# Kernel optimization log

Measured on AMD Instinct MI355X. Metric: run time of the kernel, lower is better.

The kernel has to match this reference:

```python
import jax, jax.numpy as jnp
import numpy as np

N_FEAT = 64
O_FEAT = 64
REDUCTION = 16


def conv2d(x, w, pad):
    # x: NCHW, w: OIHW
    return jax.lax.conv_general_dilated(
        x, w, window_strides=(1, 1), padding=[(pad, pad), (pad, pad)],
        dimension_numbers=('NCHW', 'OIHW', 'NCHW'))


def bwt(x):
    # Haar-like wavelet decompose: [B,C,H,W] -> [B,8C,H/2,W/2]
    x01 = x[:, :, 0::2, :] / 2
    x02 = x[:, :, 1::2, :] / 2
    x1 = x01[:, :, :, 0::2]
    x2 = x02[:, :, :, 0::2]
    x3 = x01[:, :, :, 1::2]
    x4 = x02[:, :, :, 1::2]
    x_LL = x1 + x2 + x3 + x4
    x_HL = -x1 - x2 + x3 + x4
    x_LH = -x1 + x2 - x3 + x4
    x_HH = x1 - x2 - x3 + x4
    x_HD = x1 + x2 - x3 - x4
    x_LV = -x1 + x2 + x3 - x4
    x_LD = x1 - x2 + x3 - x4
    x_HV = -x1 - x2 - x3 - x4
    return jnp.concatenate((x_LL, x_HL, x_LH, x_HH, x_HD, x_LV, x_LD, x_HV), axis=1)


def ibwt(x):
    # [B,8C,h,w] -> [B,C,2h,2w]
    B, C8, h, w = x.shape
    C = C8 // 8
    xs = [x[:, i * C:(i + 1) * C] / 2 for i in range(8)]
    x1, x2, x3, x4, x5, x6, x7, x8 = xs
    a00 = x1 - x2 - x3 + x4 + x5 - x6 + x7 - x8  # h[0::2, 0::2]
    a10 = x1 - x2 + x3 - x4 - x5 + x6 - x7 + x8  # h[1::2, 0::2]
    a01 = x1 + x2 - x3 - x4 - x5 - x6 + x7 + x8  # h[0::2, 1::2]
    a11 = x1 + x2 + x3 + x4 + x5 + x6 + x7 + x8  # h[1::2, 1::2]
    # interleave columns then rows
    even_rows = jnp.stack([a00, a01], axis=-1).reshape(B, C, h, 2 * w)
    odd_rows = jnp.stack([a10, a11], axis=-1).reshape(B, C, h, 2 * w)
    return jnp.stack([even_rows, odd_rows], axis=-2).reshape(B, C, 2 * h, 2 * w)


def sal(x, w_sal):
    max_pool = jnp.max(x, axis=1, keepdims=True)
    avg_pool = jnp.mean(x, axis=1, keepdims=True)
    channel_pool = jnp.concatenate([max_pool, avg_pool], axis=1)
    y = jax.nn.sigmoid(conv2d(channel_pool, w_sal, pad=2))
    return x * y


def cal(x, w_ca1, w_ca2):
    y = jnp.mean(x, axis=(2, 3), keepdims=True)  # adaptive avg pool to 1x1
    y = jax.nn.relu(conv2d(y, w_ca1, pad=0))
    y = jax.nn.sigmoid(conv2d(y, w_ca2, pad=0))
    return x * y


def setup_inputs() -> dict:
    key = jax.random.key(0)
    ks = jax.random.split(key, 10)
    n, o, r = N_FEAT, O_FEAT, REDUCTION
    s = 0.05
    return {
        'x': jax.random.normal(ks[0], (4, n, 256, 256), dtype=jnp.float32),
        'w_body1': jax.random.normal(ks[1], (n, 8 * n, 3, 3), dtype=jnp.float32) * s,
        'w_body2': jax.random.normal(ks[2], (8 * n, n, 3, 3), dtype=jnp.float32) * s,
        'w_sal': jax.random.normal(ks[3], (1, 2, 5, 5), dtype=jnp.float32) * s,
        'w_ca1': jax.random.normal(ks[4], (8 * n // r, 8 * n, 1, 1), dtype=jnp.float32) * s,
        'w_ca2': jax.random.normal(ks[5], (8 * n, 8 * n // r, 1, 1), dtype=jnp.float32) * s,
        'w_1x1': jax.random.normal(ks[6], (8 * n, 8 * n, 1, 1), dtype=jnp.float32) * s,
        'w_3x3': jax.random.normal(ks[7], (o, n, 3, 3), dtype=jnp.float32) * s,
        'w_final': jax.random.normal(ks[8], (o, n, 1, 1), dtype=jnp.float32) * s,
    }


def reference(x, w_body1, w_body2, w_sal, w_ca1, w_ca2, w_1x1, w_3x3, w_final):
    residual = x
    x_bwt = bwt(x)                               # [B, 8n, H/2, W/2]
    res = conv2d(x_bwt, w_body1, pad=1)          # body: conv-act-conv
    res = jax.nn.relu(res)
    res = conv2d(res, w_body2, pad=1)
    res = sal(res, w_sal)
    res = cal(res, w_ca1, w_ca2)
    res = conv2d(res, w_1x1, pad=0) + x_bwt
    wavelet_path = ibwt(res)                     # [B, n, H, W]
    out = jax.nn.relu(conv2d(wavelet_path, w_3x3, pad=1))
    out = out + conv2d(residual, w_final, pad=0)
    return out
```

## Files before the change

kernel.cpp:

```cpp
#include <hip/hip_runtime.h>
#include <hip/hip_bf16.h>

typedef __hip_bfloat16 bf16;
using short8  = __attribute__((ext_vector_type(8))) short;
using floatx4 = __attribute__((ext_vector_type(4))) float;

__device__ __forceinline__ float b2f(bf16 v) { return __bfloat162float(v); }
__device__ __forceinline__ bf16 f2b(float v) { return __float2bfloat16(v); }
__device__ __forceinline__ float s2f(short s) {
    return __uint_as_float(((unsigned)(unsigned short)s) << 16);
}
__device__ __forceinline__ unsigned short fbits(float v) {
    bf16 b = f2b(v);
    return *(unsigned short*)&b;
}

constexpr int H = 256, W = 256, Hh = 128, Wh = 128, C8 = 512;
constexpr int HWh = Hh * Wh;
constexpr int HWf = H * W;
constexpr int ICP = 40;

template<int OC, int IC>
__global__ __launch_bounds__(256) void prep_wr(const float* __restrict__ w, bf16* __restrict__ wr) {
    int idx = blockIdx.x * 256 + threadIdx.x;
    if (idx >= 9 * OC * IC) return;
    int ic = idx & (IC - 1);
    int oc = (idx / IC) & (OC - 1);
    int tap = idx / (IC * OC);
    wr[idx] = f2b(w[(oc * IC + ic) * 9 + tap]);
}

__global__ __launch_bounds__(256) void prep_wfr(const float* __restrict__ wf, bf16* __restrict__ wfr) {
    int idx = blockIdx.x * 256 + threadIdx.x;
    wfr[idx] = f2b(wf[idx]);
}

__global__ __launch_bounds__(256) void prep_w1s(const float* __restrict__ w1,
                                                const float* __restrict__ scale,
                                                bf16* __restrict__ w1s) {
    int idx = blockIdx.x * 256 + threadIdx.x;
    int ic = idx & 511, oc = (idx >> 9) & 511, b = idx >> 18;
    w1s[idx] = f2b(w1[oc * 512 + ic] * scale[b * 512 + ic]);
}

constexpr int XROW = 130;
__global__ __launch_bounds__(256, 2) void bwt_nhwc(const float* __restrict__ x, bf16* __restrict__ A) {
    __shared__ unsigned short sX[2 * 64 * XROW];
    int bx = blockIdx.x;
    int i = bx >> 1, j0 = (bx & 1) * 64;
    int b = blockIdx.z;
    int tid = threadIdx.x;
    for (int k = 0; k < 16; k++) {
        int e = tid + k * 256;
        int w4 = e & 31, r = (e >> 5) & 1, c = e >> 6;
        float4 v = *(const float4*)(x + (((size_t)(b * 64 + c) * H + 2 * i + r) * W) + j0 * 2 + w4 * 4);
        unsigned lo = ((unsigned)fbits(v.y) << 16) | fbits(v.x);
        unsigned hi = ((unsigned)fbits(v.w) << 16) | fbits(v.z);
        unsigned short* dst = sX + (r * 64 + c) * XROW + w4 * 4;
        *(unsigned*)(dst) = lo;
        *(unsigned*)(dst + 2) = hi;
    }
    __syncthreads();
    int c = tid & 63, wid = tid >> 6;
    for (int k = 0; k < 16; k++) {
        int jr = wid * 16 + k;
        unsigned ev = *(const unsigned*)(sX + c * XROW + jr * 2);
        unsigned od = *(const unsigned*)(sX + (64 + c) * XROW + jr * 2);
        float x1 = s2f((short)(ev & 0xffff)) * 0.5f;
        float x3 = s2f((short)(ev >> 16)) * 0.5f;
        float x2 = s2f((short)(od & 0xffff)) * 0.5f;
        float x4 = s2f((short)(od >> 16)) * 0.5f;
        float v[8];
        v[0] =  x1 + x2 + x3 + x4;
        v[1] = -x1 - x2 + x3 + x4;
        v[2] = -x1 + x2 - x3 + x4;
        v[3] =  x1 - x2 - x3 + x4;
        v[4] =  x1 + x2 - x3 - x4;
        v[5] = -x1 + x2 + x3 - x4;
        v[6] =  x1 - x2 + x3 - x4;
        v[7] = -x1 - x2 - x3 - x4;
        size_t base = ((size_t)((b * Hh + i) * Wh) + j0 + jr) * 512 + c;
        #pragma unroll
        for (int band = 0; band < 8; band++)
            A[base + band * 64] = f2b(v[band]);
    }
}

template<int IC, int OC, int HW, bool RELU, int MINW>
__global__ __launch_bounds__(256, MINW) void conv3x3_mfma(const bf16* __restrict__ in,
                                                          const bf16* __restrict__ wr,
                                                          bf16* __restrict__ out) {
    __shared__ bf16 sIn[18 * 18 * ICP];
    __shared__ bf16 sW9[9 * 64 * ICP];

    const int tilesX = HW / 16;
    int tX = (blockIdx.x % tilesX) * 16;
    int tY = (blockIdx.x / tilesX) * 16;
    int oBase = blockIdx.y * 64;
    int b = blockIdx.z;
    int tid = threadIdx.x;
    int lane = tid & 63, wid = tid >> 6;
    int m = lane & 15, quad = lane >> 4;

    floatx4 acc[4][4];
    #pragma unroll
    for (int i = 0; i < 4; i++)
        #pragma unroll
        for (int j = 0; j < 4; j++)
            acc[i][j] = (floatx4){0.f, 0.f, 0.f, 0.f};

    const bf16* inB = in + (size_t)b * HW * HW * IC;

    for (int ic0 = 0; ic0 < IC; ic0 += 32) {
        __syncthreads();
        for (int e = tid; e < 18 * 18 * 4; e += 256) {
            int q = e & 3, cell = e >> 2;
            int r = cell / 18, c = cell - r * 18;
            int gr = tY + r - 1, gc = tX + c - 1;
            short8 v = {0, 0, 0, 0, 0, 0, 0, 0};
            if (gr >= 0 && gr < HW && gc >= 0 && gc < HW)
                v = *(const short8*)(inB + (size_t)(gr * HW + gc) * IC + ic0 + q * 8);
            *(short8*)(sIn + cell * ICP + q * 8) = v;
        }
        for (int e = tid; e < 2304; e += 256) {
            int q = e & 3, row = e >> 2;
            int tap = row >> 6, oc = row & 63;
            short8 v = *(const short8*)(wr + (size_t)(tap * OC + oBase + oc) * IC + ic0 + q * 8);
            *(short8*)(sW9 + row * ICP + q * 8) = v;
        }
        __syncthreads();
        #pragma unroll
        for (int dy = 0; dy < 3; dy++) {
            #pragma unroll
            for (int dx = 0; dx < 3; dx++) {
                short8 bfr[4];
                #pragma unroll
                for (int nt = 0; nt < 4; nt++)
                    bfr[nt] = *(const short8*)(sW9 + ((dy * 3 + dx) * 64 + nt * 16 + m) * ICP + quad * 8);
                #pragma unroll
                for (int mt = 0; mt < 4; mt++) {
                    int r = wid * 4 + mt;
                    short8 afr = *(const short8*)(sIn + ((r + dy) * 18 + m + dx) * ICP + quad * 8);
                    #pragma unroll
                    for (int nt = 0; nt < 4; nt++)
                        acc[mt][nt] = __builtin_amdgcn_mfma_f32_16x16x32_bf16(afr, bfr[nt], acc[mt][nt], 0, 0, 0);
                }
            }
        }
    }
    #pragma unroll
    for (int mt = 0; mt < 4; mt++) {
        int row = tY + wid * 4 + mt;
        #pragma unroll
        for (int nt = 0; nt < 4; nt++) {
            int oc = oBase + nt * 16 + m;
            #pragma unroll
            for (int reg = 0; reg < 4; reg++) {
                int col = tX + quad * 4 + reg;
                float v = acc[mt][nt][reg];
                if (RELU) v = fmaxf(v, 0.f);
                out[((size_t)(b * HW + row) * HW + col) * OC + oc] = f2b(v);
            }
        }
    }
}

__global__ __launch_bounds__(256, 2) void conv1x1_mfma(const bf16* __restrict__ t3,
                                                       const float* __restrict__ smap,
                                                       const bf16* __restrict__ w1s,
                                                       bf16* __restrict__ A) {
    __shared__ bf16 sX[256 * ICP];
    __shared__ bf16 sW1[128 * ICP];
    int p0 = blockIdx.x * 256;
    int oBase = blockIdx.y * 128;
    int b = blockIdx.z;
    int tid = threadIdx.x;
    int lane = tid & 63, wid = tid >> 6;
    int m = lane & 15, quad = lane >> 4;
    const bf16* wB = w1s + (size_t)b * 512 * 512;
    const bf16* tB = t3 + ((size_t)b << 14) * 512;
    const float* sm = smap + (b << 14);

    floatx4 acc[4][8];
    #pragma unroll
    for (int i = 0; i < 4; i++)
        #pragma unroll
        for (int j = 0; j < 8; j++)
            acc[i][j] = (floatx4){0.f, 0.f, 0.f, 0.f};

    for (int ic0 = 0; ic0 < 512; ic0 += 32) {
        __syncthreads();
        #pragma unroll
        for (int k = 0; k < 4; k++) {
            int e = tid + k * 256;
            int q = e & 3, p = e >> 2;
            float sc = sm[p0 + p];
            short8 v = *(const short8*)(tB + (size_t)(p0 + p) * 512 + ic0 + q * 8);
            short8 o;
            #pragma unroll
            for (int t = 0; t < 8; t++)
                o[t] = (short)fbits(s2f(v[t]) * sc);
            *(short8*)(sX + p * ICP + q * 8) = o;
        }
        #pragma unroll
        for (int k = 0; k < 2; k++) {
            int e = tid + k * 256;
            int q = e & 3, oc = e >> 2;
            *(short8*)(sW1 + oc * ICP + q * 8) =
                *(const short8*)(wB + (size_t)(oBase + oc) * 512 + ic0 + q * 8);
        }
        __syncthreads();
        short8 bfr[8];
        #pragma unroll
        for (int nt = 0; nt < 8; nt++)
            bfr[nt] = *(const short8*)(sW1 + (nt * 16 + m) * ICP + quad * 8);
        #pragma unroll
        for (int mt = 0; mt < 4; mt++) {
            short8 afr = *(const short8*)(sX + ((wid * 4 + mt) * 16 + m) * ICP + quad * 8);
            #pragma unroll
            for (int nt = 0; nt < 8; nt++)
                acc[mt][nt] = __builtin_amdgcn_mfma_f32_16x16x32_bf16(afr, bfr[nt], acc[mt][nt], 0, 0, 0);
        }
    }
    bf16* AB = A + ((size_t)b << 14) * 512;
    #pragma unroll
    for (int mt = 0; mt < 4; mt++) {
        #pragma unroll
        for (int nt = 0; nt < 8; nt++) {
            int oc = oBase + nt * 16 + m;
            #pragma unroll
            for (int reg = 0; reg < 4; reg++) {
                int p = p0 + wid * 64 + mt * 16 + quad * 4 + reg;
                size_t a = (size_t)p * 512 + oc;
                AB[a] = f2b(acc[mt][nt][reg] + b2f(AB[a]));
            }
        }
    }
}

__global__ __launch_bounds__(256) void sal_pool(const bf16* __restrict__ t2, float* __restrict__ pool) {
    int pix = blockIdx.x * 4 + (threadIdx.x >> 6);
    int lane = threadIdx.x & 63;
    short8 v = *(const short8*)(t2 + (size_t)pix * 512 + lane * 8);
    float mx = -1e30f, sm = 0.f;
    #pragma unroll
    for (int i = 0; i < 8; i++) {
        float f = s2f(v[i]);
        mx = fmaxf(mx, f);
        sm += f;
    }
    #pragma unroll
    for (int off = 32; off > 0; off >>= 1) {
        mx = fmaxf(mx, __shfl_xor(mx, off));
        sm += __shfl_xor(sm, off);
    }
    if (lane == 0) {
        int b = pix >> 14, px = pix & (HWh - 1);
        pool[((size_t)(b * 2) << 14) + px] = mx;
        pool[((size_t)(b * 2 + 1) << 14) + px] = sm * (1.f / 512.f);
    }
}

__global__ __launch_bounds__(256) void sal_conv(const float* __restrict__ pool,
                                                const float* __restrict__ wsal,
                                                float* __restrict__ smap) {
    int p = blockIdx.x * 256 + threadIdx.x;
    int b = p >> 14, px = p & (HWh - 1);
    int iy = px >> 7, ix = px & 127;
    float acc = 0.f;
    #pragma unroll
    for (int ch = 0; ch < 2; ch++)
        #pragma unroll
        for (int dy = 0; dy < 5; dy++)
            #pragma unroll
            for (int dx = 0; dx < 5; dx++) {
                int gy = iy + dy - 2, gx = ix + dx - 2;
                if (gy >= 0 && gy < Hh && gx >= 0 && gx < Wh)
                    acc += pool[((size_t)(b * 2 + ch) << 14) + gy * Wh + gx] *
                           wsal[ch * 25 + dy * 5 + dx];
            }
    smap[p] = 1.f / (1.f + expf(-acc));
}

__global__ __launch_bounds__(256) void sal_wsum(const bf16* __restrict__ t2,
                                                const float* __restrict__ smap,
                                                float* __restrict__ chsum) {
    int b = blockIdx.y;
    int p0 = blockIdx.x * 32;
    int t = threadIdx.x;
    float s0 = 0.f, s1 = 0.f;
    const bf16* tB = t2 + ((size_t)b << 14) * 512;
    #pragma unroll 4
    for (int k = 0; k < 32; k++) {
        int pix = p0 + k;
        float sc = smap[(b << 14) + pix];
        unsigned v = *(const unsigned*)(tB + (size_t)pix * 512 + 2 * t);
        s0 += s2f((short)(v & 0xffff)) * sc;
        s1 += s2f((short)(v >> 16)) * sc;
    }
    atomicAdd(&chsum[b * 512 + 2 * t], s0);
    atomicAdd(&chsum[b * 512 + 2 * t + 1], s1);
}

__global__ __launch_bounds__(512) void cal_kernel(const float* __restrict__ chsum,
                                                  const float* __restrict__ wca1,
                                                  const float* __restrict__ wca2,
                                                  float* __restrict__ scale) {
    int b = blockIdx.x;
    __shared__ float sMean[512];
    __shared__ float sH[32];
    sMean[threadIdx.x] = chsum[b * C8 + threadIdx.x] * (1.f / 16384.f);
    __syncthreads();
    if (threadIdx.x < 32) {
        float a = 0.f;
        for (int cc = 0; cc < 512; cc++)
            a += wca1[threadIdx.x * 512 + cc] * sMean[cc];
        sH[threadIdx.x] = fmaxf(a, 0.f);
    }
    __syncthreads();
    float a = 0.f;
    #pragma unroll
    for (int j = 0; j < 32; j++)
        a += wca2[threadIdx.x * 32 + j] * sH[j];
    scale[b * C8 + threadIdx.x] = 1.f / (1.f + expf(-a));
}

__global__ __launch_bounds__(256) void ibwt_nhwc(const bf16* __restrict__ A, bf16* __restrict__ E) {
    int idx = blockIdx.x * 256 + threadIdx.x;
    int c = idx & 63;
    int j = (idx >> 6) & 127;
    int i = (idx >> 13) & 127;
    int b = idx >> 20;
    size_t base = (size_t)(idx >> 6) * 512 + c;
    float xs[8];
    #pragma unroll
    for (int k = 0; k < 8; k++)
        xs[k] = b2f(A[base + k * 64]) * 0.5f;
    float a00 = xs[0] - xs[1] - xs[2] + xs[3] + xs[4] - xs[5] + xs[6] - xs[7];
    float a10 = xs[0] - xs[1] + xs[2] - xs[3] - xs[4] + xs[5] - xs[6] + xs[7];
    float a01 = xs[0] + xs[1] - xs[2] - xs[3] - xs[4] - xs[5] + xs[6] + xs[7];
    float a11 = xs[0] + xs[1] + xs[2] + xs[3] + xs[4] + xs[5] + xs[6] + xs[7];
    bf16* Ep = E + ((size_t)((b * H + 2 * i) * W + 2 * j)) * 64 + c;
    Ep[0]           = f2b(a00);
    Ep[64]          = f2b(a01);
    Ep[W * 64]      = f2b(a10);
    Ep[W * 64 + 64] = f2b(a11);
}

__global__ __launch_bounds__(256, 2) void final_mfma(const bf16* __restrict__ E,
                                                     const bf16* __restrict__ wr3,
                                                     const float* __restrict__ x,
                                                     const bf16* __restrict__ wfr,
                                                     float* __restrict__ out) {
    __shared__ bf16 sIn[18 * 18 * ICP];
    __shared__ bf16 sW9[9 * 64 * ICP];
    const int tilesX = W / 16;
    int tX = (blockIdx.x % tilesX) * 16;
    int tY = (blockIdx.x / tilesX) * 16;
    int b = blockIdx.z;
    int tid = threadIdx.x;
    int lane = tid & 63, wid = tid >> 6;
    int m = lane & 15, quad = lane >> 4;

    floatx4 acc[4][4];
    #pragma unroll
    for (int i = 0; i < 4; i++)
        #pragma unroll
        for (int j = 0; j < 4; j++)
            acc[i][j] = (floatx4){0.f, 0.f, 0.f, 0.f};

    const bf16* inB = E + (size_t)b * HWf * 64;
    for (int ic0 = 0; ic0 < 64; ic0 += 32) {
        __syncthreads();
        for (int e = tid; e < 18 * 18 * 4; e += 256) {
            int q = e & 3, cell = e >> 2;
            int r = cell / 18, c = cell - r * 18;
            int gr = tY + r - 1, gc = tX + c - 1;
            short8 v = {0, 0, 0, 0, 0, 0, 0, 0};
            if (gr >= 0 && gr < H && gc >= 0 && gc < W)
                v = *(const short8*)(inB + (size_t)(gr * W + gc) * 64 + ic0 + q * 8);
            *(short8*)(sIn + cell * ICP + q * 8) = v;
        }
        for (int e = tid; e < 2304; e += 256) {
            int q = e & 3, row = e >> 2;
            int tap = row >> 6, oc = row & 63;
            short8 v = *(const short8*)(wr3 + (size_t)(tap * 64 + oc) * 64 + ic0 + q * 8);
            *(short8*)(sW9 + row * ICP + q * 8) = v;
        }
        __syncthreads();
        #pragma unroll
        for (int dy = 0; dy < 3; dy++) {
            #pragma unroll
            for (int dx = 0; dx < 3; dx++) {
                short8 bfr[4];
                #pragma unroll
                for (int nt = 0; nt < 4; nt++)
                    bfr[nt] = *(const short8*)(sW9 + ((dy * 3 + dx) * 64 + nt * 16 + m) * ICP + quad * 8);
                #pragma unroll
                for (int mt = 0; mt < 4; mt++) {
                    int r = wid * 4 + mt;
                    short8 afr = *(const short8*)(sIn + ((r + dy) * 18 + m + dx) * ICP + quad * 8);
                    #pragma unroll
                    for (int nt = 0; nt < 4; nt++)
                        acc[mt][nt] = __builtin_amdgcn_mfma_f32_16x16x32_bf16(afr, bfr[nt], acc[mt][nt], 0, 0, 0);
                }
            }
        }
    }
    #pragma unroll
    for (int i = 0; i < 4; i++)
        #pragma unroll
        for (int j = 0; j < 4; j++)
            #pragma unroll
            for (int r = 0; r < 4; r++)
                acc[i][j][r] = fmaxf(acc[i][j][r], 0.f);

    for (int icc = 0; icc < 64; icc += 32) {
        __syncthreads();
        for (int e = tid; e < 2048; e += 256) {
            int c4 = e & 3, r = (e >> 2) & 15, ic = e >> 6;
            float4 v = *(const float4*)(x + ((size_t)(b * 64 + icc + ic) * H + tY + r) * W + tX + c4 * 4);
            bf16* dst = sIn + ((r + 1) * 18 + c4 * 4 + 1) * ICP + ic;
            dst[0]       = f2b(v.x);
            dst[ICP]     = f2b(v.y);
            dst[2 * ICP] = f2b(v.z);
            dst[3 * ICP] = f2b(v.w);
        }
        {
            int q = tid & 3, oc = tid >> 2;
            *(short8*)(sW9 + (64 + oc) * ICP + q * 8) =
                *(const short8*)(wfr + oc * 64 + icc + q * 8);
        }
        __syncthreads();
        short8 bfr[4];
        #pragma unroll
        for (int nt = 0; nt < 4; nt++)
            bfr[nt] = *(const short8*)(sW9 + (64 + nt * 16 + m) * ICP + quad * 8);
        #pragma unroll
        for (int mt = 0; mt < 4; mt++) {
            int r = wid * 4 + mt;
            short8 afr = *(const short8*)(sIn + ((r + 1) * 18 + m + 1) * ICP + quad * 8);
            #pragma unroll
            for (int nt = 0; nt < 4; nt++)
                acc[mt][nt] = __builtin_amdgcn_mfma_f32_16x16x32_bf16(afr, bfr[nt], acc[mt][nt], 0, 0, 0);
        }
    }
    #pragma unroll
    for (int mt = 0; mt < 4; mt++) {
        int gr = tY + wid * 4 + mt;
        #pragma unroll
        for (int nt = 0; nt < 4; nt++) {
            int oc = nt * 16 + m;
            *(floatx4*)(out + ((size_t)(b * 64 + oc) * H + gr) * W + tX + quad * 4) = acc[mt][nt];
        }
    }
}

extern "C" void kernel_launch(void* const* d_in, const int* in_sizes, int n_in,
                              void* d_out, int out_size, void* d_ws, size_t ws_size,
                              hipStream_t stream) {
    const float* x       = (const float*)d_in[0];
    const float* w_body1 = (const float*)d_in[1];
    const float* w_body2 = (const float*)d_in[2];
    const float* w_sal   = (const float*)d_in[3];
    const float* w_ca1   = (const float*)d_in[4];
    const float* w_ca2   = (const float*)d_in[5];
    const float* w_1x1   = (const float*)d_in[6];
    const float* w_3x3   = (const float*)d_in[7];
    const float* w_final = (const float*)d_in[8];

    char* ws = (char*)d_ws;
    bf16*  A     = (bf16*)(ws + 0);
    bf16*  T2    = (bf16*)(ws + 67108864);
    bf16*  T1    = (bf16*)(ws + 134217728);
    float* pool  = (float*)(ws + 134217728);
    float* smap  = (float*)(ws + 134742016);
    float* chsum = (float*)(ws + 135004160);
    float* scale = (float*)(ws + 135012352);
    bf16*  w1s   = (bf16*)(ws + 135020544);
    bf16*  wr3   = (bf16*)(ws + 137117696);
    bf16*  wfr   = (bf16*)(ws + 137191424);
    bf16*  E     = T2;
    bf16*  wr1   = (bf16*)d_out;
    bf16*  wr2   = (bf16*)((char*)d_out + 589824);

    prep_wr<64, 512><<<1152, 256, 0, stream>>>(w_body1, wr1);
    prep_wr<512, 64><<<1152, 256, 0, stream>>>(w_body2, wr2);
    bwt_nhwc<<<dim3(256, 1, 4), 256, 0, stream>>>(x, A);
    conv3x3_mfma<512, 64, 128, true, 1><<<dim3(64, 1, 4), 256, 0, stream>>>(A, wr1, T1);
    conv3x3_mfma<64, 512, 128, false, 2><<<dim3(64, 8, 4), 256, 0, stream>>>(T1, wr2, T2);
    sal_pool<<<16384, 256, 0, stream>>>(T2, pool);
    sal_conv<<<256, 256, 0, stream>>>(pool, w_sal, smap);
    hipMemsetAsync(chsum, 0, 4 * 512 * sizeof(float), stream);
    sal_wsum<<<dim3(512, 4), 256, 0, stream>>>(T2, smap, chsum);
    cal_kernel<<<4, 512, 0, stream>>>(chsum, w_ca1, w_ca2, scale);
    prep_w1s<<<4096, 256, 0, stream>>>(w_1x1, scale, w1s);
    prep_wr<64, 64><<<144, 256, 0, stream>>>(w_3x3, wr3);
    prep_wfr<<<16, 256, 0, stream>>>(w_final, wfr);
    conv1x1_mfma<<<dim3(64, 4, 4), 256, 0, stream>>>(T2, smap, w1s, A);
    ibwt_nhwc<<<16384, 256, 0, stream>>>(A, E);
    final_mfma<<<dim3(256, 1, 4), 256, 0, stream>>>(E, wr3, x, wfr, (float*)d_out);
}
```

Baseline: 478.7 us.

## Pre-swizzle weights into MFMA fragment order and double-buffer activation tiles

Weights are repacked into per-lane MFMA B-fragment layout so conv kernels read them straight from global/L2 instead of staging them in shared memory. Activation tiles are double-buffered, with register prefetch of the next K chunk overlapping the MFMA work, and A-fragment rows are reused across the dy taps. The first conv moves to 8-row tiles for more blocks, and the spatial-attention scale in the 1x1 conv moves from the input to the output epilogue. In exchange, weight fragments come from cache every iteration and register pressure goes up.

```diff
diff --git a/kernel.cpp b/kernel.cpp
--- a/kernel.cpp
+++ b/kernel.cpp
@@ -21,26 +21,47 @@
 constexpr int ICP = 40;
 
 template<int OC, int IC>
-__global__ __launch_bounds__(256) void prep_wr(const float* __restrict__ w, bf16* __restrict__ wr) {
+__global__ __launch_bounds__(256) void prep_wrT(const float* __restrict__ w, bf16* __restrict__ wrT) {
     int idx = blockIdx.x * 256 + threadIdx.x;
     if (idx >= 9 * OC * IC) return;
-    int ic = idx & (IC - 1);
-    int oc = (idx / IC) & (OC - 1);
-    int tap = idx / (IC * OC);
-    wr[idx] = f2b(w[(oc * IC + ic) * 9 + tap]);
-}
-
-__global__ __launch_bounds__(256) void prep_wfr(const float* __restrict__ wf, bf16* __restrict__ wfr) {
+    constexpr int G = OC / 64, KC = IC / 32;
+    int j = idx & 7;
+    int l = (idx >> 3) & 63;
+    int nt = (idx >> 9) & 3;
+    int rest = idx >> 11;
+    int g = rest % G;
+    int rest2 = rest / G;
+    int kc = rest2 % KC;
+    int tap = rest2 / KC;
+    int oc = g * 64 + nt * 16 + (l & 15);
+    int ic = kc * 32 + (l >> 4) * 8 + j;
+    wrT[idx] = f2b(w[(oc * IC + ic) * 9 + tap]);
+}
+
+__global__ __launch_bounds__(256) void prep_w1sT(const float* __restrict__ w1,
+                                                 const float* __restrict__ scale,
+                                                 bf16* __restrict__ w1sT) {
     int idx = blockIdx.x * 256 + threadIdx.x;
-    wfr[idx] = f2b(wf[idx]);
-}
-
-__global__ __launch_bounds__(256) void prep_w1s(const float* __restrict__ w1,
-                                                const float* __restrict__ scale,
-                                                bf16* __restrict__ w1s) {
+    int j = idx & 7;
+    int l = (idx >> 3) & 63;
+    int nt = (idx >> 9) & 7;
+    int g = (idx >> 12) & 3;
+    int kc = (idx >> 14) & 15;
+    int b = idx >> 18;
+    int oc = g * 128 + nt * 16 + (l & 15);
+    int ic = kc * 32 + (l >> 4) * 8 + j;
+    w1sT[idx] = f2b(w1[oc * 512 + ic] * scale[b * 512 + ic]);
+}
+
+__global__ __launch_bounds__(256) void prep_wfrT(const float* __restrict__ wf, bf16* __restrict__ wfrT) {
     int idx = blockIdx.x * 256 + threadIdx.x;
-    int ic = idx & 511, oc = (idx >> 9) & 511, b = idx >> 18;
-    w1s[idx] = f2b(w1[oc * 512 + ic] * scale[b * 512 + ic]);
+    int j = idx & 7;
+    int l = (idx >> 3) & 63;
+    int nt = (idx >> 9) & 3;
+    int kc = idx >> 11;
+    int oc = nt * 16 + (l & 15);
+    int ic = kc * 32 + (l >> 4) * 8 + j;
+    wfrT[idx] = f2b(wf[oc * 64 + ic]);
 }
 
 constexpr int XROW = 130;
@@ -86,74 +107,98 @@
     }
 }
 
-template<int IC, int OC, int HW, bool RELU, int MINW>
-__global__ __launch_bounds__(256, MINW) void conv3x3_mfma(const bf16* __restrict__ in,
-                                                          const bf16* __restrict__ wr,
-                                                          bf16* __restrict__ out) {
-    __shared__ bf16 sIn[18 * 18 * ICP];
-    __shared__ bf16 sW9[9 * 64 * ICP];
+template<int IC, int OC, int HW, int TR, bool RELU>
+__global__ __launch_bounds__(256, 2) void conv3x3_mfma(const bf16* __restrict__ in,
+                                                       const bf16* __restrict__ wrT,
+                                                       bf16* __restrict__ out) {
+    constexpr int MT = TR / 4, NKC = IC / 32, G = OC / 64;
+    constexpr int CELLS = (TR + 2) * 18;
+    constexpr int NLD = (CELLS * 4 + 255) / 256;
+    __shared__ bf16 sIn[2][CELLS * ICP];
 
     const int tilesX = HW / 16;
     int tX = (blockIdx.x % tilesX) * 16;
-    int tY = (blockIdx.x / tilesX) * 16;
-    int oBase = blockIdx.y * 64;
+    int tY = (blockIdx.x / tilesX) * TR;
+    int g = blockIdx.y;
     int b = blockIdx.z;
     int tid = threadIdx.x;
     int lane = tid & 63, wid = tid >> 6;
     int m = lane & 15, quad = lane >> 4;
 
-    floatx4 acc[4][4];
-    #pragma unroll
-    for (int i = 0; i < 4; i++)
+    floatx4 acc[MT][4];
+    #pragma unroll
+    for (int i = 0; i < MT; i++)
         #pragma unroll
         for (int j = 0; j < 4; j++)
             acc[i][j] = (floatx4){0.f, 0.f, 0.f, 0.f};
 
     const bf16* inB = in + (size_t)b * HW * HW * IC;
 
-    for (int ic0 = 0; ic0 < IC; ic0 += 32) {
+    auto load_tile = [&](int kc, short8* tmp) {
+        #pragma unroll
+        for (int k = 0; k < NLD; k++) {
+            int e = tid + k * 256;
+            tmp[k] = (short8){0, 0, 0, 0, 0, 0, 0, 0};
+            if (e < CELLS * 4) {
+                int q = e & 3, cell = e >> 2;
+                int r = cell / 18, c = cell - r * 18;
+                int gr = tY + r - 1, gc = tX + c - 1;
+                if (gr >= 0 && gr < HW && gc >= 0 && gc < HW)
+                    tmp[k] = *(const short8*)(inB + (size_t)(gr * HW + gc) * IC + kc * 32 + q * 8);
+            }
+        }
+    };
+    auto write_tile = [&](int buf, short8* tmp) {
+        #pragma unroll
+        for (int k = 0; k < NLD; k++) {
+            int e = tid + k * 256;
+            if (e < CELLS * 4) {
+                int q = e & 3, cell = e >> 2;
+                *(short8*)(sIn[buf] + cell * ICP + q * 8) = tmp[k];
+            }
+        }
+    };
+
+    {
+        short8 t0[NLD];
+        load_tile(0, t0);
+        write_tile(0, t0);
+    }
+    for (int kc = 0; kc < NKC; kc++) {
+        short8 nxt[NLD];
         __syncthreads();
-        for (int e = tid; e < 18 * 18 * 4; e += 256) {
-            int q = e & 3, cell = e >> 2;
-            int r = cell / 18, c = cell - r * 18;
-            int gr = tY + r - 1, gc = tX + c - 1;
-            short8 v = {0, 0, 0, 0, 0, 0, 0, 0};
-            if (gr >= 0 && gr < HW && gc >= 0 && gc < HW)
-                v = *(const short8*)(inB + (size_t)(gr * HW + gc) * IC + ic0 + q * 8);
-            *(short8*)(sIn + cell * ICP + q * 8) = v;
-        }
-        for (int e = tid; e < 2304; e += 256) {
-            int q = e & 3, row = e >> 2;
-            int tap = row >> 6, oc = row & 63;
-            short8 v = *(const short8*)(wr + (size_t)(tap * OC + oBase + oc) * IC + ic0 + q * 8);
-            *(short8*)(sW9 + row * ICP + q * 8) = v;
-        }
-        __syncthreads();
-        #pragma unroll
-        for (int dy = 0; dy < 3; dy++) {
-            #pragma unroll
-            for (int dx = 0; dx < 3; dx++) {
+        bool pf = (kc + 1 < NKC);
+        if (pf) load_tile(kc + 1, nxt);
+        const bf16* sbuf = sIn[kc & 1];
+        #pragma unroll
+        for (int dx = 0; dx < 3; dx++) {
+            short8 arow[MT + 2];
+            #pragma unroll
+            for (int i = 0; i < MT + 2; i++)
+                arow[i] = *(const short8*)(sbuf + ((wid * MT + i) * 18 + m + dx) * ICP + quad * 8);
+            #pragma unroll
+            for (int dy = 0; dy < 3; dy++) {
+                int tap = dy * 3 + dx;
+                const bf16* wt = wrT + ((size_t)((tap * NKC + kc) * G + g) * 4) * 512;
                 short8 bfr[4];
                 #pragma unroll
                 for (int nt = 0; nt < 4; nt++)
-                    bfr[nt] = *(const short8*)(sW9 + ((dy * 3 + dx) * 64 + nt * 16 + m) * ICP + quad * 8);
+                    bfr[nt] = *(const short8*)(wt + nt * 512 + lane * 8);
                 #pragma unroll
-                for (int mt = 0; mt < 4; mt++) {
-                    int r = wid * 4 + mt;
-                    short8 afr = *(const short8*)(sIn + ((r + dy) * 18 + m + dx) * ICP + quad * 8);
+                for (int mt = 0; mt < MT; mt++)
                     #pragma unroll
                     for (int nt = 0; nt < 4; nt++)
-                        acc[mt][nt] = __builtin_amdgcn_mfma_f32_16x16x32_bf16(afr, bfr[nt], acc[mt][nt], 0, 0, 0);
-                }
-            }
-        }
-    }
-    #pragma unroll
-    for (int mt = 0; mt < 4; mt++) {
-        int row = tY + wid * 4 + mt;
+                        acc[mt][nt] = __builtin_amdgcn_mfma_f32_16x16x32_bf16(arow[mt + dy], bfr[nt], acc[mt][nt], 0, 0, 0);
+            }
+        }
+        if (pf) write_tile((kc + 1) & 1, nxt);
+    }
+    #pragma unroll
+    for (int mt = 0; mt < MT; mt++) {
+        int row = tY + wid * MT + mt;
         #pragma unroll
         for (int nt = 0; nt < 4; nt++) {
-            int oc = oBase + nt * 16 + m;
+            int oc = g * 64 + nt * 16 + m;
             #pragma unroll
             for (int reg = 0; reg < 4; reg++) {
                 int col = tX + quad * 4 + reg;
@@ -167,17 +212,15 @@
 
 __global__ __launch_bounds__(256, 2) void conv1x1_mfma(const bf16* __restrict__ t3,
                                                        const float* __restrict__ smap,
-                                                       const bf16* __restrict__ w1s,
+                                                       const bf16* __restrict__ w1sT,
                                                        bf16* __restrict__ A) {
-    __shared__ bf16 sX[256 * ICP];
-    __shared__ bf16 sW1[128 * ICP];
+    __shared__ bf16 sX[2][256 * ICP];
     int p0 = blockIdx.x * 256;
-    int oBase = blockIdx.y * 128;
+    int gB = blockIdx.y;
     int b = blockIdx.z;
     int tid = threadIdx.x;
     int lane = tid & 63, wid = tid >> 6;
     int m = lane & 15, quad = lane >> 4;
-    const bf16* wB = w1s + (size_t)b * 512 * 512;
     const bf16* tB = t3 + ((size_t)b << 14) * 512;
     const float* sm = smap + (b << 14);
 
@@ -188,51 +231,61 @@
         for (int j = 0; j < 8; j++)
             acc[i][j] = (floatx4){0.f, 0.f, 0.f, 0.f};
 
-    for (int ic0 = 0; ic0 < 512; ic0 += 32) {
+    auto load_x = [&](int kc, short8* tmp) {
+        #pragma unroll
+        for (int k = 0; k < 4; k++) {
+            int e = tid + k * 256;
+            int q = e & 3, p = e >> 2;
+            tmp[k] = *(const short8*)(tB + (size_t)(p0 + p) * 512 + kc * 32 + q * 8);
+        }
+    };
+    auto write_x = [&](int buf, short8* tmp) {
+        #pragma unroll
+        for (int k = 0; k < 4; k++) {
+            int e = tid + k * 256;
+            int q = e & 3, p = e >> 2;
+            *(short8*)(sX[buf] + p * ICP + q * 8) = tmp[k];
+        }
+    };
+
+    {
+        short8 t0[4];
+        load_x(0, t0);
+        write_x(0, t0);
+    }
+    for (int kc = 0; kc < 16; kc++) {
+        short8 nxt[4];
         __syncthreads();
-        #pragma unroll
-        for (int k = 0; k < 4; k++) {
-            int e = tid + k * 256;
-            int q = e & 3, p = e >> 2;
-            float sc = sm[p0 + p];
-            short8 v = *(const short8*)(tB + (size_t)(p0 + p) * 512 + ic0 + q * 8);
-            short8 o;
-            #pragma unroll
-            for (int t = 0; t < 8; t++)
-                o[t] = (short)fbits(s2f(v[t]) * sc);
-            *(short8*)(sX + p * ICP + q * 8) = o;
-        }
-        #pragma unroll
-        for (int k = 0; k < 2; k++) {
-            int e = tid + k * 256;
-            int q = e & 3, oc = e >> 2;
-            *(short8*)(sW1 + oc * ICP + q * 8) =
-                *(const short8*)(wB + (size_t)(oBase + oc) * 512 + ic0 + q * 8);
-        }
-        __syncthreads();
+        bool pf = (kc + 1 < 16);
+        if (pf) load_x(kc + 1, nxt);
+        const bf16* sbuf = sX[kc & 1];
+        const bf16* wt = w1sT + ((size_t)((b * 16 + kc) * 4 + gB) * 8) * 512;
         short8 bfr[8];
         #pragma unroll
         for (int nt = 0; nt < 8; nt++)
-            bfr[nt] = *(const short8*)(sW1 + (nt * 16 + m) * ICP + quad * 8);
+            bfr[nt] = *(const short8*)(wt + nt * 512 + lane * 8);
         #pragma unroll
         for (int mt = 0; mt < 4; mt++) {
-            short8 afr = *(const short8*)(sX + ((wid * 4 + mt) * 16 + m) * ICP + quad * 8);
+            short8 afr = *(const short8*)(sbuf + ((wid * 4 + mt) * 16 + m) * ICP + quad * 8);
             #pragma unroll
             for (int nt = 0; nt < 8; nt++)
                 acc[mt][nt] = __builtin_amdgcn_mfma_f32_16x16x32_bf16(afr, bfr[nt], acc[mt][nt], 0, 0, 0);
         }
+        if (pf) write_x((kc + 1) & 1, nxt);
     }
     bf16* AB = A + ((size_t)b << 14) * 512;
     #pragma unroll
     for (int mt = 0; mt < 4; mt++) {
+        float smv[4];
+        *(float4*)smv = *(const float4*)(sm + p0 + wid * 64 + mt * 16 + quad * 4);
         #pragma unroll
         for (int nt = 0; nt < 8; nt++) {
-            int oc = oBase + nt * 16 + m;
+            int oc = gB * 128 + nt * 16 + m;
             #pragma unroll
             for (int reg = 0; reg < 4; reg++) {
                 int p = p0 + wid * 64 + mt * 16 + quad * 4 + reg;
                 size_t a = (size_t)p * 512 + oc;
-                AB[a] = f2b(acc[mt][nt][reg] + b2f(AB[a]));
+                AB[a] = f2b(acc[mt][nt][reg] * smv[reg] + b2f(AB[a]));
             }
         }
     }
@@ -348,12 +401,12 @@
 }
 
 __global__ __launch_bounds__(256, 2) void final_mfma(const bf16* __restrict__ E,
-                                                     const bf16* __restrict__ wr3,
+                                                     const bf16* __restrict__ wr3T,
                                                      const float* __restrict__ x,
-                                                     const bf16* __restrict__ wfr,
+                                                     const bf16* __restrict__ wfrT,
                                                      float* __restrict__ out) {
-    __shared__ bf16 sIn[18 * 18 * ICP];
-    __shared__ bf16 sW9[9 * 64 * ICP];
+    constexpr int CELLS = 18 * 18;
+    __shared__ bf16 sIn[2][CELLS * ICP];
     const int tilesX = W / 16;
     int tX = (blockIdx.x % tilesX) * 16;
     int tY = (blockIdx.x / tilesX) * 16;
@@ -370,81 +423,123 @@
             acc[i][j] = (floatx4){0.f, 0.f, 0.f, 0.f};
 
     const bf16* inB = E + (size_t)b * HWf * 64;
-    for (int ic0 = 0; ic0 < 64; ic0 += 32) {
-        __syncthreads();
-        for (int e = tid; e < 18 * 18 * 4; e += 256) {
-            int q = e & 3, cell = e >> 2;
-            int r = cell / 18, c = cell - r * 18;
-            int gr = tY + r - 1, gc = tX + c - 1;
-            short8 v = {0, 0, 0, 0, 0, 0, 0, 0};
-            if (gr >= 0 && gr < H && gc >= 0 && gc < W)
-                v = *(const short8*)(inB + (size_t)(gr * W + gc) * 64 + ic0 + q * 8);
-            *(short8*)(sIn + cell * ICP + q * 8) = v;
-        }
-        for (int e = tid; e < 2304; e += 256) {
-            int q = e & 3, row = e >> 2;
-            int tap = row >> 6, oc = row & 63;
-            short8 v = *(const short8*)(wr3 + (size_t)(tap * 64 + oc) * 64 + ic0 + q * 8);
-            *(short8*)(sW9 + row * ICP + q * 8) = v;
-        }
-        __syncthreads();
-        #pragma unroll
-        for (int dy = 0; dy < 3; dy++) {
-            #pragma unroll
-            for (int dx = 0; dx < 3; dx++) {
+
+    auto load_e = [&](int kc, short8* tmp) {
+        #pragma unroll
+        for (int k = 0; k < 6; k++) {
+            int e = tid + k * 256;
+            tmp[k] = (short8){0, 0, 0, 0, 0, 0, 0, 0};
+            if (e < CELLS * 4) {
+                int q = e & 3, cell = e >> 2;
+                int r = cell / 18, c = cell - r * 18;
+                int gr = tY + r - 1, gc = tX + c - 1;
+                if (gr >= 0 && gr < H && gc >= 0 && gc < W)
+                    tmp[k] = *(const short8*)(inB + (size_t)(gr * W + gc) * 64 + kc * 32 + q * 8);
+            }
+        }
+    };
+    auto write_e = [&](int buf, short8* tmp) {
+        #pragma unroll
+        for (int k = 0; k < 6; k++) {
+            int e = tid + k * 256;
+            if (e < CELLS * 4) {
+                int q = e & 3, cell = e >> 2;
+                *(short8*)(sIn[buf] + cell * ICP + q * 8) = tmp[k];
+            }
+        }
+    };
+    auto compute_e = [&](int kc, int buf) {
+        const bf16* sbuf = sIn[buf];
+        #pragma unroll
+        for (int dx = 0; dx < 3; dx++) {
+            short8 arow[6];
+            #pragma unroll
+            for (int i = 0; i < 6; i++)
+                arow[i] = *(const short8*)(sbuf + ((wid * 4 + i) * 18 + m + dx) * ICP + quad * 8);
+            #pragma unroll
+            for (int dy = 0; dy < 3; dy++) {
+                int tap = dy * 3 + dx;
+                const bf16* wt = wr3T + ((size_t)(tap * 2 + kc) * 4) * 512;
                 short8 bfr[4];
                 #pragma unroll
                 for (int nt = 0; nt < 4; nt++)
-                    bfr[nt] = *(const short8*)(sW9 + ((dy * 3 + dx) * 64 + nt * 16 + m) * ICP + quad * 8);
+                    bfr[nt] = *(const short8*)(wt + nt * 512 + lane * 8);
                 #pragma unroll
-                for (int mt = 0; mt < 4; mt++) {
-                    int r = wid * 4 + mt;
-                    short8 afr = *(const short8*)(sIn + ((r + dy) * 18 + m + dx) * ICP + quad * 8);
+                for (int mt = 0; mt < 4; mt++)
                     #pragma unroll
                     for (int nt = 0; nt < 4; nt++)
-                        acc[mt][nt] = __builtin_amdgcn_mfma_f32_16x16x32_bf16(afr, bfr[nt], acc[mt][nt], 0, 0, 0);
-                }
-            }
-        }
-    }
-    #pragma unroll
-    for (int i = 0; i < 4; i++)
-        #pragma unroll
-        for (int j = 0; j < 4; j++)
-            #pragma unroll
-            for (int r = 0; r < 4; r++)
-                acc[i][j][r] = fmaxf(acc[i][j][r], 0.f);
-
-    for (int icc = 0; icc < 64; icc += 32) {
-        __syncthreads();
-        for (int e = tid; e < 2048; e += 256) {
+                        acc[mt][nt] = __builtin_amdgcn_mfma_f32_16x16x32_bf16(arow[mt + dy], bfr[nt], acc[mt][nt], 0, 0, 0);
+            }
+        }
+    };
+    auto load_xx = [&](int kc, float4* xt) {
+        #pragma unroll
+        for (int k = 0; k < 8; k++) {
+            int e = tid + k * 256;
             int c4 = e & 3, r = (e >> 2) & 15, ic = e >> 6;
-            float4 v = *(const float4*)(x + ((size_t)(b * 64 + icc + ic) * H + tY + r) * W + tX + c4 * 4);
-            bf16* dst = sIn + ((r + 1) * 18 + c4 * 4 + 1) * ICP + ic;
-            dst[0]       = f2b(v.x);
-            dst[ICP]     = f2b(v.y);
-            dst[2 * ICP] = f2b(v.z);
-            dst[3 * ICP] = f2b(v.w);
-        }
-        {
-            int q = tid & 3, oc = tid >> 2;
-            *(short8*)(sW9 + (64 + oc) * ICP + q * 8) =
-                *(const short8*)(wfr + oc * 64 + icc + q * 8);
-        }
-        __syncthreads();
+            xt[k] = *(const float4*)(x + ((size_t)(b * 64 + kc * 32 + ic) * H + tY + r) * W + tX + c4 * 4);
+        }
+    };
+    auto write_xx = [&](int buf, float4* xt) {
+        #pragma unroll
+        for (int k = 0; k < 8; k++) {
+            int e = tid + k * 256;
+            int c4 = e & 3, r = (e >> 2) & 15, ic = e >> 6;
+            bf16* dst = sIn[buf] + ((r + 1) * 18 + c4 * 4 + 1) * ICP + ic;
+            dst[0]       = f2b(xt[k].x);
+            dst[ICP]     = f2b(xt[k].y);
+            dst[2 * ICP] = f2b(xt[k].z);
+            dst[3 * ICP] = f2b(xt[k].w);
+        }
+    };
+    auto compute_x = [&](int kc, int buf) {
+        const bf16* wt = wfrT + (size_t)(kc * 4) * 512;
         short8 bfr[4];
         #pragma unroll
         for (int nt = 0; nt < 4; nt++)
-            bfr[nt] = *(const short8*)(sW9 + (64 + nt * 16 + m) * ICP + quad * 8);
+            bfr[nt] = *(const short8*)(wt + nt * 512 + lane * 8);
         #pragma unroll
         for (int mt = 0; mt < 4; mt++) {
-            int r = wid * 4 + mt;
-            short8 afr = *(const short8*)(sIn + ((r + 1) * 18 + m + 1) * ICP + quad * 8);
+            short8 afr = *(const short8*)(sIn[buf] + ((wid * 4 + mt + 1) * 18 + m + 1) * ICP + quad * 8);
             #pragma unroll
             for (int nt = 0; nt < 4; nt++)
                 acc[mt][nt] = __builtin_amdgcn_mfma_f32_16x16x32_bf16(afr, bfr[nt], acc[mt][nt], 0, 0, 0);
         }
-    }
+    };
+
+    {
+        short8 t0[6];
+        load_e(0, t0);
+        write_e(0, t0);
+        load_e(1, t0);
+        write_e(1, t0);
+    }
+    __syncthreads();
+    compute_e(0, 0);
+    __syncthreads();
+    {
+        float4 xt[8];
+        load_xx(0, xt);
+        compute_e(1, 1);
+        #pragma unroll
+        for (int i = 0; i < 4; i++)
+            #pragma unroll
+            for (int j = 0; j < 4; j++)
+                #pragma unroll
+                for (int r = 0; r < 4; r++)
+                    acc[i][j][r] = fmaxf(acc[i][j][r], 0.f);
+        write_xx(0, xt);
+    }
+    __syncthreads();
+    {
+        float4 xt[8];
+        load_xx(1, xt);
+        compute_x(0, 0);
+        write_xx(1, xt);
+    }
+    __syncthreads();
+    compute_x(1, 1);
+
     #pragma unroll
     for (int mt = 0; mt < 4; mt++) {
         int gr = tY + wid * 4 + mt;
@@ -477,27 +572,27 @@
     float* smap  = (float*)(ws + 134742016);
     float* chsum = (float*)(ws + 135004160);
     float* scale = (float*)(ws + 135012352);
-    bf16*  w1s   = (bf16*)(ws + 135020544);
-    bf16*  wr3   = (bf16*)(ws + 137117696);
-    bf16*  wfr   = (bf16*)(ws + 137191424);
+    bf16*  w1sT  = (bf16*)(ws + 135020544);
+    bf16*  wr3T  = (bf16*)(ws + 137117696);
+    bf16*  wfrT  = (bf16*)(ws + 137191424);
     bf16*  E     = T2;
-    bf16*  wr1   = (bf16*)d_out;
-    bf16*  wr2   = (bf16*)((char*)d_out + 589824);
-
-    prep_wr<64, 512><<<1152, 256, 0, stream>>>(w_body1, wr1);
-    prep_wr<512, 64><<<1152, 256, 0, stream>>>(w_body2, wr2);
+    bf16*  wr1T  = (bf16*)d_out;
+    bf16*  wr2T  = (bf16*)((char*)d_out + 589824);
+
+    prep_wrT<64, 512><<<1152, 256, 0, stream>>>(w_body1, wr1T);
+    prep_wrT<512, 64><<<1152, 256, 0, stream>>>(w_body2, wr2T);
     bwt_nhwc<<<dim3(256, 1, 4), 256, 0, stream>>>(x, A);
-    conv3x3_mfma<512, 64, 128, true, 1><<<dim3(64, 1, 4), 256, 0, stream>>>(A, wr1, T1);
-    conv3x3_mfma<64, 512, 128, false, 2><<<dim3(64, 8, 4), 256, 0, stream>>>(T1, wr2, T2);
+    conv3x3_mfma<512, 64, 128, 8, true ><<<dim3(128, 1, 4), 256, 0, stream>>>(A, wr1T, T1);
+    conv3x3_mfma<64, 512, 128, 16, false><<<dim3(64, 8, 4), 256, 0, stream>>>(T1, wr2T, T2);
     sal_pool<<<16384, 256, 0, stream>>>(T2, pool);
     sal_conv<<<256, 256, 0, stream>>>(pool, w_sal, smap);
     hipMemsetAsync(chsum, 0, 4 * 512 * sizeof(float), stream);
     sal_wsum<<<dim3(512, 4), 256, 0, stream>>>(T2, smap, chsum);
     cal_kernel<<<4, 512, 0, stream>>>(chsum, w_ca1, w_ca2, scale);
-    prep_w1s<<<4096, 256, 0, stream>>>(w_1x1, scale, w1s);
-    prep_wr<64, 64><<<144, 256, 0, stream>>>(w_3x3, wr3);
-    prep_wfr<<<16, 256, 0, stream>>>(w_final, wfr);
-    conv1x1_mfma<<<dim3(64, 4, 4), 256, 0, stream>>>(T2, smap, w1s, A);
+    prep_w1sT<<<4096, 256, 0, stream>>>(w_1x1, scale, w1sT);
+    prep_wrT<64, 64><<<144, 256, 0, stream>>>(w_3x3, wr3T);
+    prep_wfrT<<<16, 256, 0, stream>>>(w_final, wfrT);
+    conv1x1_mfma<<<dim3(64, 4, 4), 256, 0, stream>>>(T2, smap, w1sT, A);
     ibwt_nhwc<<<16384, 256, 0, stream>>>(A, E);
-    final_mfma<<<dim3(256, 1, 4), 256, 0, stream>>>(E, wr3, x, wfr, (float*)d_out);
-}
+    final_mfma<<<dim3(256, 1, 4), 256, 0, stream>>>(E, wr3T, x, wfrT, (float*)d_out);
+}
```

Measured after the change: 445.2 us. 1.08x faster.
